# Optimization experiments

Hardware: AMD Instinct MI355X
Metric: run time of the kernel (lower is better)

## Reference

```python
import jax, jax.numpy as jnp
import numpy as np

NUM_NODES = 50000
NUM_REL_ORIG = 5            # original relation types
NUM_REL = 2 * NUM_REL_ORIG + 1  # augmented: original + inverse + self-loop = 11
F_IN = 128
F_OUT = 128
NUM_EDGES = 800000


def setup_inputs() -> dict:
    key = jax.random.key(0)
    k1, k2, k3, k4, k5, k6 = jax.random.split(key, 6)
    src = jax.random.randint(k1, (NUM_EDGES,), 0, NUM_NODES, dtype=jnp.int32)
    rel = jax.random.randint(k2, (NUM_EDGES,), 0, NUM_REL_ORIG, dtype=jnp.int32)
    dst = jax.random.randint(k3, (NUM_EDGES,), 0, NUM_NODES, dtype=jnp.int32)
    graph = jnp.stack([src, rel, dst], axis=1)  # [E, 3] = (head, relation, tail)
    features = jax.random.normal(k4, (NUM_NODES, F_IN), dtype=jnp.float32)
    # RGCNConv parameters (no basis/block decomposition, bias=False, root_weight=True)
    glorot = lambda k, shape: jax.random.normal(k, shape, dtype=jnp.float32) * jnp.sqrt(2.0 / (shape[-2] + shape[-1]))
    weight = glorot(k5, (NUM_REL, F_IN, F_OUT))  # per-relation weights
    root = glorot(k6, (F_IN, F_OUT))             # root (self) weight
    return {"graph": graph, "features": features, "weight": weight, "root": root}


def reference(graph, features, weight, root):
    N = features.shape[0]
    R = weight.shape[0]
    n_orig = (R - 1) // 2
    src, rel, dst = graph[:, 0], graph[:, 1], graph[:, 2]
    loop = jnp.arange(N, dtype=graph.dtype)
    # augmented edge list: original, inverse, self-loops
    full_src = jnp.concatenate([src, dst, loop])
    full_dst = jnp.concatenate([dst, src, loop])
    full_rel = jnp.concatenate([rel, rel + n_orig, jnp.full((N,), 2 * n_orig, dtype=graph.dtype)])
    # per-(relation, dst-node) mean of source features (PyG RGCNConv aggr='mean'
    # aggregates raw x_j per relation, then applies W_r to the aggregate)
    seg = full_rel * N + full_dst  # [E_full]
    msgs = features[full_src]      # [E_full, F_in] gather
    sums = jax.ops.segment_sum(msgs, seg, num_segments=R * N)           # [R*N, F_in]
    cnts = jax.ops.segment_sum(jnp.ones((seg.shape[0],), features.dtype), seg, num_segments=R * N)
    mean = sums / jnp.maximum(cnts, 1.0)[:, None]
    mean = mean.reshape(R, N, -1)  # [R, N, F_in]
    # out = sum_r mean_r @ W_r + x @ W_root
    out = jnp.einsum('rnf,rfo->no', mean, weight) + features @ root
    return out
```

## Files before the change

kernel.cpp:

```cpp
#include <hip/hip_runtime.h>
#include <hip/hip_bf16.h>

#define NN 50000
#define RO 5
#define RT 11
#define FF 128
#define EE 800000
#define EE2 (2 * EE)
#define NBINS (2 * RO * NN)
#define SLOTS 16
#define DPB 32
#define FILL_BLKS (EE2 / 256)
#define FEAT_BLKS ((NN * FF / 4) / 256)
#define WT_BLKS ((RT * FF * FF) / 256)

typedef unsigned short u16;
typedef unsigned int u32;
typedef __attribute__((ext_vector_type(4))) unsigned short u16x4;
typedef __attribute__((ext_vector_type(4))) unsigned int u32x4;
typedef __attribute__((ext_vector_type(8))) short bf16x8;
typedef __attribute__((ext_vector_type(4))) float f32x4;

__device__ __forceinline__ u16 f2b(float x) {
  unsigned u = __float_as_uint(x);
  return (u16)((u + 0x7fffu + ((u >> 16) & 1u)) >> 16);
}

__global__ __launch_bounds__(256) void pf_k(const int* __restrict__ g,
                                            const float* __restrict__ f,
                                            const float* __restrict__ w,
                                            const float* __restrict__ root,
                                            int* __restrict__ cur,
                                            u16* __restrict__ eidx,
                                            u16* __restrict__ fb,
                                            u16* __restrict__ wt) {
  const int b = blockIdx.x;
  if (b < FILL_BLKS) {
    const int m = b * 256 + threadIdx.x;
    int e, bin; u16 val;
    if (m < EE) {
      e = m;
      int s = g[3 * e], r = g[3 * e + 1], d = g[3 * e + 2];
      bin = r * NN + d; val = (u16)s;
    } else {
      e = m - EE;
      int d2 = g[3 * e], r = g[3 * e + 1], s2 = g[3 * e + 2];
      bin = (r + RO) * NN + d2; val = (u16)s2;
    }
    int pos = atomicAdd(&cur[bin], 1);
    if (pos < SLOTS) eidx[bin * SLOTS + pos] = val;
  } else if (b < FILL_BLKS + FEAT_BLKS) {
    int i = (b - FILL_BLKS) * 256 + threadIdx.x;
    float4 v = reinterpret_cast<const float4*>(f)[i];
    u16x4 o;
    o.x = f2b(v.x); o.y = f2b(v.y); o.z = f2b(v.z); o.w = f2b(v.w);
    reinterpret_cast<u16x4*>(fb)[i] = o;
  } else if (b < FILL_BLKS + FEAT_BLKS + WT_BLKS) {
    int idx = (b - FILL_BLKS - FEAT_BLKS) * 256 + threadIdx.x;
    int r = idx >> 14;
    int rem = idx & 16383;
    int k = rem >> 7;
    int o = rem & 127;
    float v = w[idx];
    if (r == 10) v += root[rem];
    int chunk = (k >> 3) ^ (o & 7);
    wt[(r << 14) + (o << 7) + (chunk << 3) + (k & 7)] = f2b(v);
  } else {
    if (threadIdx.x < 64) reinterpret_cast<u32*>(fb)[NN * 64 + threadIdx.x] = 0;
  }
}

#define ACCX(p) { a0 += __uint_as_float((p).x << 16); a1 += __uint_as_float((p).x & 0xffff0000u); \
                  a2 += __uint_as_float((p).y << 16); a3 += __uint_as_float((p).y & 0xffff0000u); \
                  a4 += __uint_as_float((p).z << 16); a5 += __uint_as_float((p).z & 0xffff0000u); \
                  a6 += __uint_as_float((p).w << 16); a7 += __uint_as_float((p).w & 0xffff0000u); }
#define ACCY(p) { b0 += __uint_as_float((p).x << 16); b1 += __uint_as_float((p).x & 0xffff0000u); \
                  b2 += __uint_as_float((p).y << 16); b3 += __uint_as_float((p).y & 0xffff0000u); \
                  b4 += __uint_as_float((p).z << 16); b5 += __uint_as_float((p).z & 0xffff0000u); \
                  b6 += __uint_as_float((p).w << 16); b7 += __uint_as_float((p).w & 0xffff0000u); }

__global__ __launch_bounds__(256) void mg_k(const int* __restrict__ cnt,
                                            const u32* __restrict__ eidx32,
                                            const u32x4* __restrict__ fv4,
                                            const u16* __restrict__ fbf,
                                            const u16* __restrict__ wt,
                                            float* __restrict__ out) {
  __shared__ __align__(16) u32x4 Asw[DPB * 16];
  const int tid  = threadIdx.x;
  const int lane = tid & 63;
  const int wv   = tid >> 6;
  const int l15  = lane & 15;
  const int ko   = lane >> 4;
  const int qid  = wv * 4 + ko;
  const int q16  = ko << 4;
  const int base = blockIdx.x * DPB;

  f32x4 acc[2][2];
#pragma unroll
  for (int i = 0; i < 2; ++i)
#pragma unroll
    for (int j = 0; j < 2; ++j) acc[i][j] = (f32x4){0.f, 0.f, 0.f, 0.f};

  const int row0 = qid * 2, row1 = row0 + 1;
  const int d0 = base + row0, d1 = base + row1;
  const bool v0 = d0 < NN, v1 = d1 < NN;

  for (int r = 0; r < 10; ++r) {
    const int seg0 = v0 ? r * NN + d0 : 0;
    const int seg1 = v1 ? r * NN + d1 : 0;
    const int c0 = v0 ? min(cnt[seg0], SLOTS) : 0;
    const int c1 = v1 ? min(cnt[seg1], SLOTS) : 0;
    const u32 sl0 = eidx32[seg0 * 8 + (l15 & 7)];
    const u32 sl1 = eidx32[seg1 * 8 + (l15 & 7)];
    int cmax = max(c0, c1);
    cmax = max(cmax, __shfl_xor(cmax, 16));
    cmax = max(cmax, __shfl_xor(cmax, 32));

    float a0 = 0.f, a1 = 0.f, a2 = 0.f, a3 = 0.f, a4 = 0.f, a5 = 0.f, a6 = 0.f, a7 = 0.f;
    float b0 = 0.f, b1 = 0.f, b2 = 0.f, b3 = 0.f, b4 = 0.f, b5 = 0.f, b6 = 0.f, b7 = 0.f;

    for (int i = 0; i < cmax; i += 4) {
      u32 wa0 = __shfl(sl0, q16 + (i >> 1));
      u32 wa1 = __shfl(sl0, q16 + (i >> 1) + 1);
      u32 wb0 = __shfl(sl1, q16 + (i >> 1));
      u32 wb1 = __shfl(sl1, q16 + (i >> 1) + 1);
      int s0 = (i     < c0) ? (int)(wa0 & 0xffffu) : NN;
      int s1 = (i + 1 < c0) ? (int)(wa0 >> 16)     : NN;
      int s2 = (i + 2 < c0) ? (int)(wa1 & 0xffffu) : NN;
      int s3 = (i + 3 < c0) ? (int)(wa1 >> 16)     : NN;
      int t0 = (i     < c1) ? (int)(wb0 & 0xffffu) : NN;
      int t1 = (i + 1 < c1) ? (int)(wb0 >> 16)     : NN;
      int t2 = (i + 2 < c1) ? (int)(wb1 & 0xffffu) : NN;
      int t3 = (i + 3 < c1) ? (int)(wb1 >> 16)     : NN;
      u32x4 p0 = fv4[s0 * 16 + l15];
      u32x4 p1 = fv4[s1 * 16 + l15];
      u32x4 p2 = fv4[s2 * 16 + l15];
      u32x4 p3 = fv4[s3 * 16 + l15];
      u32x4 p4 = fv4[t0 * 16 + l15];
      u32x4 p5 = fv4[t1 * 16 + l15];
      u32x4 p6 = fv4[t2 * 16 + l15];
      u32x4 p7 = fv4[t3 * 16 + l15];
      ACCX(p0); ACCX(p1); ACCX(p2); ACCX(p3);
      ACCY(p4); ACCY(p5); ACCY(p6); ACCY(p7);
    }

    const float i0 = (c0 > 0) ? 1.0f / (float)c0 : 0.0f;
    const float i1 = (c1 > 0) ? 1.0f / (float)c1 : 0.0f;
    u32x4 m0, m1;
    m0.x = (u32)f2b(a0 * i0) | ((u32)f2b(a1 * i0) << 16);
    m0.y = (u32)f2b(a2 * i0) | ((u32)f2b(a3 * i0) << 16);
    m0.z = (u32)f2b(a4 * i0) | ((u32)f2b(a5 * i0) << 16);
    m0.w = (u32)f2b(a6 * i0) | ((u32)f2b(a7 * i0) << 16);
    m1.x = (u32)f2b(b0 * i1) | ((u32)f2b(b1 * i1) << 16);
    m1.y = (u32)f2b(b2 * i1) | ((u32)f2b(b3 * i1) << 16);
    m1.z = (u32)f2b(b4 * i1) | ((u32)f2b(b5 * i1) << 16);
    m1.w = (u32)f2b(b6 * i1) | ((u32)f2b(b7 * i1) << 16);
    Asw[row0 * 16 + (l15 ^ (row0 & 7))] = m0;
    Asw[row1 * 16 + (l15 ^ (row1 & 7))] = m1;
    __syncthreads();

    const u16* wb = wt + (r << 14);
#pragma unroll
    for (int kc = 0; kc < 4; ++kc) {
      bf16x8 afr[2];
#pragma unroll
      for (int fq = 0; fq < 2; ++fq) {
        const int arow = fq * 16 + l15;
        afr[fq] = *reinterpret_cast<const bf16x8*>(
            &Asw[arow * 16 + ((kc * 4 + ko) ^ (arow & 7))]);
      }
#pragma unroll
      for (int fr = 0; fr < 2; ++fr) {
        const int o = wv * 32 + fr * 16 + l15;
        bf16x8 b = *reinterpret_cast<const bf16x8*>(
            wb + (o << 7) + (((kc * 4 + ko) ^ (o & 7)) << 3));
        acc[0][fr] = __builtin_amdgcn_mfma_f32_16x16x32_bf16(afr[0], b, acc[0][fr], 0, 0, 0);
        acc[1][fr] = __builtin_amdgcn_mfma_f32_16x16x32_bf16(afr[1], b, acc[1][fr], 0, 0, 0);
      }
    }
    __syncthreads();
  }

  {
    const u16* wb = wt + (10 << 14);
#pragma unroll
    for (int kc = 0; kc < 4; ++kc) {
      bf16x8 afr[2];
#pragma unroll
      for (int fq = 0; fq < 2; ++fq) {
        int rowg = base + fq * 16 + l15;
        rowg = (rowg < NN) ? rowg : NN;
        afr[fq] = *reinterpret_cast<const bf16x8*>(
            fbf + (long)rowg * FF + kc * 32 + ko * 8);
      }
#pragma unroll
      for (int fr = 0; fr < 2; ++fr) {
        const int o = wv * 32 + fr * 16 + l15;
        bf16x8 b = *reinterpret_cast<const bf16x8*>(
            wb + (o << 7) + (((kc * 4 + ko) ^ (o & 7)) << 3));
        acc[0][fr] = __builtin_amdgcn_mfma_f32_16x16x32_bf16(afr[0], b, acc[0][fr], 0, 0, 0);
        acc[1][fr] = __builtin_amdgcn_mfma_f32_16x16x32_bf16(afr[1], b, acc[1][fr], 0, 0, 0);
      }
    }
  }

#pragma unroll
  for (int fq = 0; fq < 2; ++fq)
#pragma unroll
    for (int fr = 0; fr < 2; ++fr)
#pragma unroll
      for (int q2 = 0; q2 < 4; ++q2) {
        const int row = base + fq * 16 + ko * 4 + q2;
        if (row < NN) out[row * FF + wv * 32 + fr * 16 + l15] = acc[fq][fr][q2];
      }
}

extern "C" void kernel_launch(void* const* d_in, const int* in_sizes, int n_in,
                              void* d_out, int out_size, void* d_ws, size_t ws_size,
                              hipStream_t stream) {
  const int*   graph  = (const int*)d_in[0];
  const float* feat   = (const float*)d_in[1];
  const float* weight = (const float*)d_in[2];
  const float* root   = (const float*)d_in[3];
  float* out = (float*)d_out;
  char* ws = (char*)d_ws;

  u16* fbf  = (u16*)(ws);
  u16* wt   = (u16*)(ws + 12800512);
  int* cur  = (int*)(ws + 13160960);
  u16* eidx = (u16*)(ws + 15161088);

  hipMemsetAsync(cur, 0, NBINS * sizeof(int), stream);
  pf_k<<<FILL_BLKS + FEAT_BLKS + WT_BLKS + 1, 256, 0, stream>>>(
      graph, feat, weight, root, cur, eidx, fbf, wt);
  mg_k<<<(NN + DPB - 1) / DPB, 256, 0, stream>>>(cur, (const u32*)eidx,
                                                 (const u32x4*)fbf, fbf, wt, out);
}
```

Before: 289.1 us.

## Fuse memset, preprocessing and aggregation into one cooperative persistent kernel

Replaces the memset plus two kernel launches with a single cooperative kernel that uses grid-wide syncs between phases: zeroing the counters, binning edges and converting features and weights, then running grid-stride persistent tiles for the aggregation and MFMA stage. This removes two launch gaps and the inter-kernel drain. In exchange it adds two grid barriers, caps occupancy through launch bounds and a grid sized to nb*256 blocks, and the occupancy query sits on the host path.

After: 571.5 us. 97.7% more time.

```diff
diff --git a/kernel.cpp b/kernel.cpp
--- a/kernel.cpp
+++ b/kernel.cpp
@@ -1,5 +1,8 @@
 #include <hip/hip_runtime.h>
 #include <hip/hip_bf16.h>
+#include <hip/hip_cooperative_groups.h>
+
+namespace cg = cooperative_groups;
 
 #define NN 50000
 #define RO 5
@@ -10,9 +13,7 @@
 #define NBINS (2 * RO * NN)
 #define SLOTS 16
 #define DPB 32
-#define FILL_BLKS (EE2 / 256)
-#define FEAT_BLKS ((NN * FF / 4) / 256)
-#define WT_BLKS ((RT * FF * FF) / 256)
+#define NTILES ((NN + DPB - 1) / DPB)
 
 typedef unsigned short u16;
 typedef unsigned int u32;
@@ -26,17 +27,32 @@
   return (u16)((u + 0x7fffu + ((u >> 16) & 1u)) >> 16);
 }
 
-__global__ __launch_bounds__(256) void pf_k(const int* __restrict__ g,
-                                            const float* __restrict__ f,
-                                            const float* __restrict__ w,
-                                            const float* __restrict__ root,
-                                            int* __restrict__ cur,
-                                            u16* __restrict__ eidx,
-                                            u16* __restrict__ fb,
-                                            u16* __restrict__ wt) {
-  const int b = blockIdx.x;
-  if (b < FILL_BLKS) {
-    const int m = b * 256 + threadIdx.x;
+#define ACCX(p) { a0 += __uint_as_float((p).x << 16); a1 += __uint_as_float((p).x & 0xffff0000u); \
+                  a2 += __uint_as_float((p).y << 16); a3 += __uint_as_float((p).y & 0xffff0000u); \
+                  a4 += __uint_as_float((p).z << 16); a5 += __uint_as_float((p).z & 0xffff0000u); \
+                  a6 += __uint_as_float((p).w << 16); a7 += __uint_as_float((p).w & 0xffff0000u); }
+#define ACCY(p) { b0 += __uint_as_float((p).x << 16); b1 += __uint_as_float((p).x & 0xffff0000u); \
+                  b2 += __uint_as_float((p).y << 16); b3 += __uint_as_float((p).y & 0xffff0000u); \
+                  b4 += __uint_as_float((p).z << 16); b5 += __uint_as_float((p).z & 0xffff0000u); \
+                  b6 += __uint_as_float((p).w << 16); b7 += __uint_as_float((p).w & 0xffff0000u); }
+
+__global__ __launch_bounds__(256, 6) void fused_k(
+    const int* __restrict__ g, const float* __restrict__ f,
+    const float* __restrict__ w, const float* __restrict__ root,
+    int* __restrict__ cur, u16* __restrict__ eidx,
+    u16* __restrict__ fb, u16* __restrict__ wt,
+    float* __restrict__ out) {
+  __shared__ __align__(16) u32x4 Asw[DPB * 16];
+  const int tid = threadIdx.x;
+  const int gid = blockIdx.x * 256 + tid;
+  const int S   = gridDim.x * 256;
+  cg::grid_group grid = cg::this_grid();
+
+  for (int i = gid; i < NBINS; i += S) cur[i] = 0;
+  if (gid < 64) reinterpret_cast<u32*>(fb)[NN * 64 + gid] = 0;
+  grid.sync();
+
+  for (int m = gid; m < EE2; m += S) {
     int e, bin; u16 val;
     if (m < EE) {
       e = m;
@@ -49,14 +65,14 @@
     }
     int pos = atomicAdd(&cur[bin], 1);
     if (pos < SLOTS) eidx[bin * SLOTS + pos] = val;
-  } else if (b < FILL_BLKS + FEAT_BLKS) {
-    int i = (b - FILL_BLKS) * 256 + threadIdx.x;
+  }
+  for (int i = gid; i < NN * FF / 4; i += S) {
     float4 v = reinterpret_cast<const float4*>(f)[i];
     u16x4 o;
     o.x = f2b(v.x); o.y = f2b(v.y); o.z = f2b(v.z); o.w = f2b(v.w);
     reinterpret_cast<u16x4*>(fb)[i] = o;
-  } else if (b < FILL_BLKS + FEAT_BLKS + WT_BLKS) {
-    int idx = (b - FILL_BLKS - FEAT_BLKS) * 256 + threadIdx.x;
+  }
+  for (int idx = gid; idx < RT * FF * FF; idx += S) {
     int r = idx >> 14;
     int rem = idx & 16383;
     int k = rem >> 7;
@@ -65,154 +81,139 @@
     if (r == 10) v += root[rem];
     int chunk = (k >> 3) ^ (o & 7);
     wt[(r << 14) + (o << 7) + (chunk << 3) + (k & 7)] = f2b(v);
-  } else {
-    if (threadIdx.x < 64) reinterpret_cast<u32*>(fb)[NN * 64 + threadIdx.x] = 0;
-  }
-}
-
-#define ACCX(p) { a0 += __uint_as_float((p).x << 16); a1 += __uint_as_float((p).x & 0xffff0000u); \
-                  a2 += __uint_as_float((p).y << 16); a3 += __uint_as_float((p).y & 0xffff0000u); \
-                  a4 += __uint_as_float((p).z << 16); a5 += __uint_as_float((p).z & 0xffff0000u); \
-                  a6 += __uint_as_float((p).w << 16); a7 += __uint_as_float((p).w & 0xffff0000u); }
-#define ACCY(p) { b0 += __uint_as_float((p).x << 16); b1 += __uint_as_float((p).x & 0xffff0000u); \
-                  b2 += __uint_as_float((p).y << 16); b3 += __uint_as_float((p).y & 0xffff0000u); \
-                  b4 += __uint_as_float((p).z << 16); b5 += __uint_as_float((p).z & 0xffff0000u); \
-                  b6 += __uint_as_float((p).w << 16); b7 += __uint_as_float((p).w & 0xffff0000u); }
-
-__global__ __launch_bounds__(256) void mg_k(const int* __restrict__ cnt,
-                                            const u32* __restrict__ eidx32,
-                                            const u32x4* __restrict__ fv4,
-                                            const u16* __restrict__ fbf,
-                                            const u16* __restrict__ wt,
-                                            float* __restrict__ out) {
-  __shared__ __align__(16) u32x4 Asw[DPB * 16];
-  const int tid  = threadIdx.x;
+  }
+  grid.sync();
+
+  const u32* eidx32 = reinterpret_cast<const u32*>(eidx);
+  const u32x4* fv4 = reinterpret_cast<const u32x4*>(fb);
   const int lane = tid & 63;
   const int wv   = tid >> 6;
   const int l15  = lane & 15;
   const int ko   = lane >> 4;
   const int qid  = wv * 4 + ko;
   const int q16  = ko << 4;
-  const int base = blockIdx.x * DPB;
-
-  f32x4 acc[2][2];
-#pragma unroll
-  for (int i = 0; i < 2; ++i)
-#pragma unroll
-    for (int j = 0; j < 2; ++j) acc[i][j] = (f32x4){0.f, 0.f, 0.f, 0.f};
-
-  const int row0 = qid * 2, row1 = row0 + 1;
-  const int d0 = base + row0, d1 = base + row1;
-  const bool v0 = d0 < NN, v1 = d1 < NN;
-
-  for (int r = 0; r < 10; ++r) {
-    const int seg0 = v0 ? r * NN + d0 : 0;
-    const int seg1 = v1 ? r * NN + d1 : 0;
-    const int c0 = v0 ? min(cnt[seg0], SLOTS) : 0;
-    const int c1 = v1 ? min(cnt[seg1], SLOTS) : 0;
-    const u32 sl0 = eidx32[seg0 * 8 + (l15 & 7)];
-    const u32 sl1 = eidx32[seg1 * 8 + (l15 & 7)];
-    int cmax = max(c0, c1);
-    cmax = max(cmax, __shfl_xor(cmax, 16));
-    cmax = max(cmax, __shfl_xor(cmax, 32));
-
-    float a0 = 0.f, a1 = 0.f, a2 = 0.f, a3 = 0.f, a4 = 0.f, a5 = 0.f, a6 = 0.f, a7 = 0.f;
-    float b0 = 0.f, b1 = 0.f, b2 = 0.f, b3 = 0.f, b4 = 0.f, b5 = 0.f, b6 = 0.f, b7 = 0.f;
-
-    for (int i = 0; i < cmax; i += 4) {
-      u32 wa0 = __shfl(sl0, q16 + (i >> 1));
-      u32 wa1 = __shfl(sl0, q16 + (i >> 1) + 1);
-      u32 wb0 = __shfl(sl1, q16 + (i >> 1));
-      u32 wb1 = __shfl(sl1, q16 + (i >> 1) + 1);
-      int s0 = (i     < c0) ? (int)(wa0 & 0xffffu) : NN;
-      int s1 = (i + 1 < c0) ? (int)(wa0 >> 16)     : NN;
-      int s2 = (i + 2 < c0) ? (int)(wa1 & 0xffffu) : NN;
-      int s3 = (i + 3 < c0) ? (int)(wa1 >> 16)     : NN;
-      int t0 = (i     < c1) ? (int)(wb0 & 0xffffu) : NN;
-      int t1 = (i + 1 < c1) ? (int)(wb0 >> 16)     : NN;
-      int t2 = (i + 2 < c1) ? (int)(wb1 & 0xffffu) : NN;
-      int t3 = (i + 3 < c1) ? (int)(wb1 >> 16)     : NN;
-      u32x4 p0 = fv4[s0 * 16 + l15];
-      u32x4 p1 = fv4[s1 * 16 + l15];
-      u32x4 p2 = fv4[s2 * 16 + l15];
-      u32x4 p3 = fv4[s3 * 16 + l15];
-      u32x4 p4 = fv4[t0 * 16 + l15];
-      u32x4 p5 = fv4[t1 * 16 + l15];
-      u32x4 p6 = fv4[t2 * 16 + l15];
-      u32x4 p7 = fv4[t3 * 16 + l15];
-      ACCX(p0); ACCX(p1); ACCX(p2); ACCX(p3);
-      ACCY(p4); ACCY(p5); ACCY(p6); ACCY(p7);
+
+  for (int t = blockIdx.x; t < NTILES; t += gridDim.x) {
+    const int base = t * DPB;
+    f32x4 acc[2][2];
+#pragma unroll
+    for (int i = 0; i < 2; ++i)
+#pragma unroll
+      for (int j = 0; j < 2; ++j) acc[i][j] = (f32x4){0.f, 0.f, 0.f, 0.f};
+
+    const int row0 = qid * 2, row1 = row0 + 1;
+    const int d0 = base + row0, d1 = base + row1;
+    const bool v0 = d0 < NN, v1 = d1 < NN;
+
+    for (int r = 0; r < 10; ++r) {
+      const int seg0 = v0 ? r * NN + d0 : 0;
+      const int seg1 = v1 ? r * NN + d1 : 0;
+      const int c0 = v0 ? min(cur[seg0], SLOTS) : 0;
+      const int c1 = v1 ? min(cur[seg1], SLOTS) : 0;
+      const u32 sl0 = eidx32[seg0 * 8 + (l15 & 7)];
+      const u32 sl1 = eidx32[seg1 * 8 + (l15 & 7)];
+      int cmax = max(c0, c1);
+      cmax = max(cmax, __shfl_xor(cmax, 16));
+      cmax = max(cmax, __shfl_xor(cmax, 32));
+
+      float a0 = 0.f, a1 = 0.f, a2 = 0.f, a3 = 0.f, a4 = 0.f, a5 = 0.f, a6 = 0.f, a7 = 0.f;
+      float b0 = 0.f, b1 = 0.f, b2 = 0.f, b3 = 0.f, b4 = 0.f, b5 = 0.f, b6 = 0.f, b7 = 0.f;
+
+      for (int i = 0; i < cmax; i += 4) {
+        u32 wa0 = __shfl(sl0, q16 + (i >> 1));
+        u32 wa1 = __shfl(sl0, q16 + (i >> 1) + 1);
+        u32 wb0 = __shfl(sl1, q16 + (i >> 1));
+        u32 wb1 = __shfl(sl1, q16 + (i >> 1) + 1);
+        int s0 = (i     < c0) ? (int)(wa0 & 0xffffu) : NN;
+        int s1 = (i + 1 < c0) ? (int)(wa0 >> 16)     : NN;
+        int s2 = (i + 2 < c0) ? (int)(wa1 & 0xffffu) : NN;
+        int s3 = (i + 3 < c0) ? (int)(wa1 >> 16)     : NN;
+        int t0 = (i     < c1) ? (int)(wb0 & 0xffffu) : NN;
+        int t1 = (i + 1 < c1) ? (int)(wb0 >> 16)     : NN;
+        int t2 = (i + 2 < c1) ? (int)(wb1 & 0xffffu) : NN;
+        int t3 = (i + 3 < c1) ? (int)(wb1 >> 16)     : NN;
+        u32x4 p0 = fv4[s0 * 16 + l15];
+        u32x4 p1 = fv4[s1 * 16 + l15];
+        u32x4 p2 = fv4[s2 * 16 + l15];
+        u32x4 p3 = fv4[s3 * 16 + l15];
+        u32x4 p4 = fv4[t0 * 16 + l15];
+        u32x4 p5 = fv4[t1 * 16 + l15];
+        u32x4 p6 = fv4[t2 * 16 + l15];
+        u32x4 p7 = fv4[t3 * 16 + l15];
+        ACCX(p0); ACCX(p1); ACCX(p2); ACCX(p3);
+        ACCY(p4); ACCY(p5); ACCY(p6); ACCY(p7);
+      }
+
+      const float i0 = (c0 > 0) ? 1.0f / (float)c0 : 0.0f;
+      const float i1 = (c1 > 0) ? 1.0f / (float)c1 : 0.0f;
+      u32x4 m0, m1;
+      m0.x = (u32)f2b(a0 * i0) | ((u32)f2b(a1 * i0) << 16);
+      m0.y = (u32)f2b(a2 * i0) | ((u32)f2b(a3 * i0) << 16);
+      m0.z = (u32)f2b(a4 * i0) | ((u32)f2b(a5 * i0) << 16);
+      m0.w = (u32)f2b(a6 * i0) | ((u32)f2b(a7 * i0) << 16);
+      m1.x = (u32)f2b(b0 * i1) | ((u32)f2b(b1 * i1) << 16);
+      m1.y = (u32)f2b(b2 * i1) | ((u32)f2b(b3 * i1) << 16);
+      m1.z = (u32)f2b(b4 * i1) | ((u32)f2b(b5 * i1) << 16);
+      m1.w = (u32)f2b(b6 * i1) | ((u32)f2b(b7 * i1) << 16);
+      Asw[row0 * 16 + (l15 ^ (row0 & 7))] = m0;
+      Asw[row1 * 16 + (l15 ^ (row1 & 7))] = m1;
+      __syncthreads();
+
+      const u16* wb = wt + (r << 14);
+#pragma unroll
+      for (int kc = 0; kc < 4; ++kc) {
+        bf16x8 afr[2];
+#pragma unroll
+        for (int fq = 0; fq < 2; ++fq) {
+          const int arow = fq * 16 + l15;
+          afr[fq] = *reinterpret_cast<const bf16x8*>(
+              &Asw[arow * 16 + ((kc * 4 + ko) ^ (arow & 7))]);
+        }
+#pragma unroll
+        for (int fr = 0; fr < 2; ++fr) {
+          const int o = wv * 32 + fr * 16 + l15;
+          bf16x8 bfrag = *reinterpret_cast<const bf16x8*>(
+              wb + (o << 7) + (((kc * 4 + ko) ^ (o & 7)) << 3));
+          acc[0][fr] = __builtin_amdgcn_mfma_f32_16x16x32_bf16(afr[0], bfrag, acc[0][fr], 0, 0, 0);
+          acc[1][fr] = __builtin_amdgcn_mfma_f32_16x16x32_bf16(afr[1], bfrag, acc[1][fr], 0, 0, 0);
+        }
+      }
+      __syncthreads();
     }
 
-    const float i0 = (c0 > 0) ? 1.0f / (float)c0 : 0.0f;
-    const float i1 = (c1 > 0) ? 1.0f / (float)c1 : 0.0f;
-    u32x4 m0, m1;
-    m0.x = (u32)f2b(a0 * i0) | ((u32)f2b(a1 * i0) << 16);
-    m0.y = (u32)f2b(a2 * i0) | ((u32)f2b(a3 * i0) << 16);
-    m0.z = (u32)f2b(a4 * i0) | ((u32)f2b(a5 * i0) << 16);
-    m0.w = (u32)f2b(a6 * i0) | ((u32)f2b(a7 * i0) << 16);
-    m1.x = (u32)f2b(b0 * i1) | ((u32)f2b(b1 * i1) << 16);
-    m1.y = (u32)f2b(b2 * i1) | ((u32)f2b(b3 * i1) << 16);
-    m1.z = (u32)f2b(b4 * i1) | ((u32)f2b(b5 * i1) << 16);
-    m1.w = (u32)f2b(b6 * i1) | ((u32)f2b(b7 * i1) << 16);
-    Asw[row0 * 16 + (l15 ^ (row0 & 7))] = m0;
-    Asw[row1 * 16 + (l15 ^ (row1 & 7))] = m1;
-    __syncthreads();
-
-    const u16* wb = wt + (r << 14);
-#pragma unroll
-    for (int kc = 0; kc < 4; ++kc) {
-      bf16x8 afr[2];
-#pragma unroll
-      for (int fq = 0; fq < 2; ++fq) {
-        const int arow = fq * 16 + l15;
-        afr[fq] = *reinterpret_cast<const bf16x8*>(
-            &Asw[arow * 16 + ((kc * 4 + ko) ^ (arow & 7))]);
-      }
-#pragma unroll
-      for (int fr = 0; fr < 2; ++fr) {
-        const int o = wv * 32 + fr * 16 + l15;
-        bf16x8 b = *reinterpret_cast<const bf16x8*>(
-            wb + (o << 7) + (((kc * 4 + ko) ^ (o & 7)) << 3));
-        acc[0][fr] = __builtin_amdgcn_mfma_f32_16x16x32_bf16(afr[0], b, acc[0][fr], 0, 0, 0);
-        acc[1][fr] = __builtin_amdgcn_mfma_f32_16x16x32_bf16(afr[1], b, acc[1][fr], 0, 0, 0);
+    {
+      const u16* wb = wt + (10 << 14);
+#pragma unroll
+      for (int kc = 0; kc < 4; ++kc) {
+        bf16x8 afr[2];
+#pragma unroll
+        for (int fq = 0; fq < 2; ++fq) {
+          int rowg = base + fq * 16 + l15;
+          rowg = (rowg < NN) ? rowg : NN;
+          afr[fq] = *reinterpret_cast<const bf16x8*>(
+              fb + (long)rowg * FF + kc * 32 + ko * 8);
+        }
+#pragma unroll
+        for (int fr = 0; fr < 2; ++fr) {
+          const int o = wv * 32 + fr * 16 + l15;
+          bf16x8 bfrag = *reinterpret_cast<const bf16x8*>(
+              wb + (o << 7) + (((kc * 4 + ko) ^ (o & 7)) << 3));
+          acc[0][fr] = __builtin_amdgcn_mfma_f32_16x16x32_bf16(afr[0], bfrag, acc[0][fr], 0, 0, 0);
+          acc[1][fr] = __builtin_amdgcn_mfma_f32_16x16x32_bf16(afr[1], bfrag, acc[1][fr], 0, 0, 0);
+        }
       }
     }
-    __syncthreads();
-  }
-
-  {
-    const u16* wb = wt + (10 << 14);
-#pragma unroll
-    for (int kc = 0; kc < 4; ++kc) {
-      bf16x8 afr[2];
-#pragma unroll
-      for (int fq = 0; fq < 2; ++fq) {
-        int rowg = base + fq * 16 + l15;
-        rowg = (rowg < NN) ? rowg : NN;
-        afr[fq] = *reinterpret_cast<const bf16x8*>(
-            fbf + (long)rowg * FF + kc * 32 + ko * 8);
-      }
-#pragma unroll
-      for (int fr = 0; fr < 2; ++fr) {
-        const int o = wv * 32 + fr * 16 + l15;
-        bf16x8 b = *reinterpret_cast<const bf16x8*>(
-            wb + (o << 7) + (((kc * 4 + ko) ^ (o & 7)) << 3));
-        acc[0][fr] = __builtin_amdgcn_mfma_f32_16x16x32_bf16(afr[0], b, acc[0][fr], 0, 0, 0);
-        acc[1][fr] = __builtin_amdgcn_mfma_f32_16x16x32_bf16(afr[1], b, acc[1][fr], 0, 0, 0);
-      }
-    }
-  }
-
-#pragma unroll
-  for (int fq = 0; fq < 2; ++fq)
-#pragma unroll
-    for (int fr = 0; fr < 2; ++fr)
-#pragma unroll
-      for (int q2 = 0; q2 < 4; ++q2) {
-        const int row = base + fq * 16 + ko * 4 + q2;
-        if (row < NN) out[row * FF + wv * 32 + fr * 16 + l15] = acc[fq][fr][q2];
-      }
+
+#pragma unroll
+    for (int fq = 0; fq < 2; ++fq)
+#pragma unroll
+      for (int fr = 0; fr < 2; ++fr)
+#pragma unroll
+        for (int q2 = 0; q2 < 4; ++q2) {
+          const int row = base + fq * 16 + ko * 4 + q2;
+          if (row < NN) out[row * FF + wv * 32 + fr * 16 + l15] = acc[fq][fr][q2];
+        }
+  }
 }
 
 extern "C" void kernel_launch(void* const* d_in, const int* in_sizes, int n_in,
@@ -230,9 +231,13 @@
   int* cur  = (int*)(ws + 13160960);
   u16* eidx = (u16*)(ws + 15161088);
 
-  hipMemsetAsync(cur, 0, NBINS * sizeof(int), stream);
-  pf_k<<<FILL_BLKS + FEAT_BLKS + WT_BLKS + 1, 256, 0, stream>>>(
-      graph, feat, weight, root, cur, eidx, fbf, wt);
-  mg_k<<<(NN + DPB - 1) / DPB, 256, 0, stream>>>(cur, (const u32*)eidx,
-                                                 (const u32x4*)fbf, fbf, wt, out);
+  int nb = 6;
+  (void)hipOccupancyMaxActiveBlocksPerMultiprocessor(&nb, fused_k, 256, 0);
+  if (nb < 1) nb = 1;
+  if (nb > 8) nb = 8;
+  dim3 grid(nb * 256), block(256);
+
+  void* args[] = {(void*)&graph, (void*)&feat, (void*)&weight, (void*)&root,
+                  (void*)&cur, (void*)&eidx, (void*)&fbf, (void*)&wt, (void*)&out};
+  hipLaunchCooperativeKernel(fused_k, grid, block, args, 0, stream);
 }
```
